# Kernel optimization log

Hardware: AMD Instinct MI355X
Metric: run time of the kernel (lower is better)

## Reference

```python
import jax, jax.numpy as jnp
import numpy as np
from jax import lax

N_CLS = 3
ALPHA = 2
NMS = True


def _make_level(key, B, A, D, H, W, P, counts):
    k1, k2, k3, k4, k5 = jax.random.split(key, 5)
    C = N_CLS * A
    logit = jax.random.normal(k1, (B, C, D, H, W), dtype=jnp.float32)
    # valid positive coords use d,h,w >= 1 so padded writes to (0,0,0,0) never collide
    a = jax.random.randint(k2, (B, P), 0, A)
    d = jax.random.randint(k3, (B, P), 1, D)
    h = jax.random.randint(k4, (B, P), 1, H)
    w = jax.random.randint(k5, (B, P), 1, W)
    labels = jax.random.randint(jax.random.fold_in(key, 7), (B, P), 0, N_CLS)
    valid = jnp.arange(P)[None, :] < jnp.asarray(counts)[:, None]  # [B,P]
    coord = jnp.stack([a, d, h, w], axis=-1)
    coord = jnp.where(valid[..., None], coord, -1).astype(jnp.int32)
    # ground-truth prob map: -1 = negative, class id (float) at positive voxels
    prob_gt = -jnp.ones((B, A, D, H, W), dtype=jnp.float32)
    cs = jnp.where(valid[..., None], coord, 0)
    b_idx = jnp.arange(B)[:, None]
    vals = jnp.where(valid, labels.astype(jnp.float32), -1.0)
    prob_gt = prob_gt.at[b_idx, cs[..., 0], cs[..., 1], cs[..., 2], cs[..., 3]].set(vals)
    return logit, prob_gt, coord


def setup_inputs() -> dict:
    key = jax.random.key(0)
    kA, kB = jax.random.split(key)
    logit0, prob_gt0, coord0 = _make_level(kA, 4, 3, 64, 64, 64, 128, [128, 64, 32, 0])
    logit1, prob_gt1, coord1 = _make_level(kB, 4, 3, 32, 32, 32, 128, [64, 16, 8, 128])
    weight_cls = jnp.array([1.0, 1.5, 2.0], dtype=jnp.float32)
    return {
        "logit0": logit0, "logit1": logit1,
        "prob_gt0": prob_gt0, "prob_gt1": prob_gt1,
        "coord0": coord0, "coord1": coord1,
        "weight_cls": weight_cls,
    }


def _level_loss(logit, prob_gt, coord_gt, weight_cls):
    B, C, D, H, W = logit.shape
    A = C // N_CLS
    logit = logit.reshape(B, N_CLS, A, D, H, W)
    logp = jax.nn.log_softmax(logit, axis=1)
    nll = -logp                      # [B,N_cls,A,D,H,W]
    prob = jnp.exp(logp)
    nll_neg = nll[:, 0]              # [B,A,D,H,W]
    prob_neg = prob[:, 0]
    negmask = (prob_gt == -1).astype(logit.dtype)
    if NMS:
        mp = lax.reduce_window(nll_neg, -jnp.inf, lax.max,
                               (1, 1, 3, 3, 3), (1, 1, 1, 1, 1),
                               [(0, 0), (0, 0), (1, 1), (1, 1), (1, 1)])
        negmask = negmask * lax.stop_gradient((mp == nll_neg).astype(logit.dtype))
    w_neg = (1.0 - lax.stop_gradient(prob_neg)) ** ALPHA * negmask
    loss_neg = jnp.sum(nll_neg * w_neg)
    count_neg = jnp.sum(w_neg)
    # positives: ragged coord gather, masked instead of per-sample python loop
    valid = coord_gt[:, :, 0] > -1                       # [B,P]
    c = jnp.where(valid[..., None], coord_gt, 0)         # safe coords
    a, d, h, w = c[..., 0], c[..., 1], c[..., 2], c[..., 3]
    b_idx = jnp.arange(B)[:, None]
    cls = prob_gt[b_idx, a, d, h, w].astype(jnp.int32)   # class id at positives
    cls = jnp.where(valid, cls, 0)
    p_t = prob[b_idx, cls, a, d, h, w]
    nll_t = nll[b_idx, cls, a, d, h, w]
    w_pos = ((1.0 - lax.stop_gradient(p_t)) ** ALPHA
             * weight_cls[cls] * valid.astype(logit.dtype))
    loss_pos = jnp.sum(nll_t * w_pos)
    count_pos = jnp.sum(w_pos)
    return loss_pos, loss_neg, count_pos, count_neg


def reference(logit0, logit1, prob_gt0, prob_gt1, coord0, coord1, weight_cls):
    lp0, ln0, cp0, cn0 = _level_loss(logit0, prob_gt0, coord0, weight_cls)
    lp1, ln1, cp1, cn1 = _level_loss(logit1, prob_gt1, coord1, weight_cls)
    return jnp.stack([lp0 + lp1, ln0 + ln1, cp0 + cp1, cn0 + cn1])
```

## Files before the change

### kernel.cpp

```cpp
#include <hip/hip_runtime.h>
#include <math.h>

#define NEG_INF (-INFINITY)

__device__ __forceinline__ float nll3(float l0, float l1, float l2) {
    float m = fmaxf(l0, fmaxf(l1, l2));
    float e0 = __expf(l0 - m);
    float e1 = __expf(l1 - m);
    float e2 = __expf(l2 - m);
    return __logf(e0 + e1 + e2) - (l0 - m);
}

__device__ __forceinline__ float4 fmax4(float4 a, float4 b) {
    return make_float4(fmaxf(a.x, b.x), fmaxf(a.y, b.y),
                       fmaxf(a.z, b.z), fmaxf(a.w, b.w));
}

template<int W, int HT, int ZT, int D, int H>
__device__ void neg_block(int ub, int tid,
                          const float* __restrict__ logit,
                          const float* __restrict__ pg,
                          float2* __restrict__ slot,
                          float* lds, float2* red) {
    constexpr int LQ = W / 4;
    constexpr int SR = W + 4;
    constexpr int SROWS = HT + 2;
    constexpr int QS = SROWS * LQ;
    constexpr int HW = H * W;
    constexpr int ZTI = D / ZT;
    constexpr int HTI = H / HT;
    constexpr int NLL_SZ = SROWS * SR;
    constexpr int HV_OFF = 3 * NLL_SZ;
    constexpr int HV_SZ = HT * SR;

    int t = ub;
    const int ht = t % HTI; t /= HTI;
    const int zt = t % ZTI; t /= ZTI;
    const int ba = t;
    const int a = ba % 3, b = ba / 3;
    const int z0 = zt * ZT, h0 = ht * HT;

    const long S = (long)D * HW;
    const long cs = 3 * S;
    const float* lb  = logit + ((long)b * 9 + a) * S;
    const float* pgb = pg + (long)ba * S;

    const int er = tid / LQ;
    const int q  = tid % LQ;
    const int lane = tid & 63;
    const int l_er = er * SR + 4 * q;
    const int po = (h0 + er) * W + 4 * q;

    int roff[2]; bool rok[2];
#pragma unroll
    for (int r = 0; r < 2; ++r) {
        const int k = tid + 256 * r;
        const int row = k / LQ, qq = k % LQ;
        const int h = h0 - 1 + row;
        rok[r]  = (k < QS) && (h >= 0) && (h < H);
        roff[r] = min(max(h, 0), H - 1) * W + 4 * qq;
    }

    float4 rA[2][3] = {}, rB[2][3] = {};
    float4 pgA = {}, pgB = {};
    bool pvA, pvB = false;

    auto issue = [&](float4 (&rg)[2][3], int zp) -> bool {
        const bool pv = (zp >= 0) && (zp < D);
        if (pv) {
#pragma unroll
            for (int r = 0; r < 2; ++r) {
                if (tid + 256 * r < QS) {
                    const float* p = lb + (long)zp * HW + roff[r];
                    rg[r][0] = *(const float4*)p;
                    rg[r][1] = *(const float4*)(p + cs);
                    rg[r][2] = *(const float4*)(p + 2 * cs);
                }
            }
        }
        return pv;
    };

    pvA = issue(rA, z0 - 1);

    float loss = 0.f, cnt = 0.f;

#pragma unroll
    for (int zi = 0; zi <= ZT + 1; ++zi) {
        const int zc = z0 - 1 + zi;
        if (zi <= ZT) pvB = issue(rB, zc + 1);
        if (zi >= 1 && zi <= ZT)
            pgB = *(const float4*)(pgb + (long)zc * HW + po);

        {
            float* nb = lds + (zi % 3) * NLL_SZ;
#pragma unroll
            for (int r = 0; r < 2; ++r) {
                const int k = tid + 256 * r;
                if (k < QS) {
                    const int row = k / LQ, qq = k % LQ;
                    const bool ok = pvA && rok[r];
                    float4 n;
                    n.x = ok ? nll3(rA[r][0].x, rA[r][1].x, rA[r][2].x) : NEG_INF;
                    n.y = ok ? nll3(rA[r][0].y, rA[r][1].y, rA[r][2].y) : NEG_INF;
                    n.z = ok ? nll3(rA[r][0].z, rA[r][1].z, rA[r][2].z) : NEG_INF;
                    n.w = ok ? nll3(rA[r][0].w, rA[r][1].w, rA[r][2].w) : NEG_INF;
                    *(float4*)(nb + row * SR + 4 * qq) = n;
                }
            }
        }
        __syncthreads();

        {
            const float* nb = lds + (zi % 3) * NLL_SZ;
            float* hb = lds + HV_OFF + (zi % 3) * HV_SZ;
            float4 v0 = *(const float4*)(nb + l_er);
            float4 v1 = *(const float4*)(nb + l_er + SR);
            float4 v2 = *(const float4*)(nb + l_er + 2 * SR);
            float4 vm = fmax4(v0, fmax4(v1, v2));
            float le = __shfl(vm.w, lane - 1);
            float re = __shfl(vm.x, lane + 1);
            le = (q == 0)      ? NEG_INF : le;
            re = (q == LQ - 1) ? NEG_INF : re;
            float4 hv;
            hv.x = fmaxf(le,   fmaxf(vm.x, vm.y));
            hv.y = fmaxf(vm.x, fmaxf(vm.y, vm.z));
            hv.z = fmaxf(vm.y, fmaxf(vm.z, vm.w));
            hv.w = fmaxf(vm.z, fmaxf(vm.w, re));
            *(float4*)(hb + l_er) = hv;
        }
        __syncthreads();

        if (zi >= 2) {
            const float* nbm = lds + ((zi - 1) % 3) * NLL_SZ;
            const float* hb0 = lds + HV_OFF + ((zi - 2) % 3) * HV_SZ;
            const float* hb1 = lds + HV_OFF + ((zi - 1) % 3) * HV_SZ;
            const float* hb2 = lds + HV_OFF + (zi % 3) * HV_SZ;
            float4 nc = *(const float4*)(nbm + l_er + SR);
            float4 m  = fmax4(*(const float4*)(hb0 + l_er),
                        fmax4(*(const float4*)(hb1 + l_er),
                              *(const float4*)(hb2 + l_er)));
            const float pgv[4] = {pgA.x, pgA.y, pgA.z, pgA.w};
            const float ncv[4] = {nc.x, nc.y, nc.z, nc.w};
            const float mv[4]  = {m.x, m.y, m.z, m.w};
#pragma unroll
            for (int i = 0; i < 4; ++i) {
                if (pgv[i] == -1.0f && mv[i] == ncv[i]) {
                    float pn = __expf(-ncv[i]);
                    float wn = (1.f - pn) * (1.f - pn);
                    loss += ncv[i] * wn;
                    cnt  += wn;
                }
            }
        }

        pvA = pvB;
#pragma unroll
        for (int r = 0; r < 2; ++r)
#pragma unroll
            for (int c = 0; c < 3; ++c) rA[r][c] = rB[r][c];
        pgA = pgB;
    }

#pragma unroll
    for (int off = 32; off > 0; off >>= 1) {
        loss += __shfl_down(loss, off);
        cnt  += __shfl_down(cnt, off);
    }
    if (lane == 0) red[tid >> 6] = make_float2(loss, cnt);
    __syncthreads();
    if (tid == 0) {
        float sx = 0.f, sy = 0.f;
#pragma unroll
        for (int i = 0; i < 4; ++i) { sx += red[i].x; sy += red[i].y; }
        *slot = make_float2(sx, sy);
    }
}

__device__ void pos_wave8(int sub, int lane,
                          const float* __restrict__ logit,
                          const float* __restrict__ prob_gt,
                          const int* __restrict__ coord,
                          const float* __restrict__ wcls,
                          float2* __restrict__ slot,
                          int D, int H, int W) {
    const int A = 3, P = 128;
    const long S = (long)D * H * W;
    const int i = sub * 64 + lane;
    const int b = i / P;
    const int* c = coord + (long)i * 4;
    const int a = c[0];
    float loss = 0.f, cnt = 0.f;
    if (a > -1) {
        const int d = c[1], h = c[2], w = c[3];
        const long s = ((long)d * H + h) * W + w;
        const int cls = (int)prob_gt[((long)b * A + a) * S + s];
        const float* lp = logit + ((long)b * 3 * A + a) * S + s;
        float l0 = lp[0];
        float l1 = lp[(long)A * S];
        float l2 = lp[2L * A * S];
        float m = fmaxf(l0, fmaxf(l1, l2));
        float e0 = __expf(l0 - m);
        float e1 = __expf(l1 - m);
        float e2 = __expf(l2 - m);
        float lsum = __logf(e0 + e1 + e2);
        float lc = (cls == 0) ? l0 : ((cls == 1) ? l1 : l2);
        float lpc = (lc - m) - lsum;
        float pt = __expf(lpc);
        float wp = (1.f - pt) * (1.f - pt) * wcls[cls];
        loss = (-lpc) * wp;
        cnt = wp;
    }
#pragma unroll
    for (int off = 32; off > 0; off >>= 1) {
        loss += __shfl_down(loss, off);
        cnt  += __shfl_down(cnt, off);
    }
    if (lane == 0) *slot = make_float2(loss, cnt);
}

#define NB0 768
#define NB1 96
#define NBNEG (NB0 + NB1)
#define NBP 4
#define TOTAL_BLOCKS (NBNEG + NBP)
#define NWP 16

__global__ __launch_bounds__(256)
void mega_kernel(const float* __restrict__ logit0,
                 const float* __restrict__ logit1,
                 const float* __restrict__ pg0,
                 const float* __restrict__ pg1,
                 const int* __restrict__ coord0,
                 const int* __restrict__ coord1,
                 const float* __restrict__ wcls,
                 float2* __restrict__ ws) {
    __shared__ float lds[7128];
    __shared__ float2 red[4];
    const int bid = blockIdx.x;
    const int tid = threadIdx.x;
    float2* wsneg = ws;
    float2* wspos = ws + NBNEG;
    if (bid < NB0) {
        neg_block<64, 16, 4, 64, 64>(bid, tid, logit0, pg0, wsneg + bid, lds, red);
    } else if (bid < NBNEG) {
        neg_block<32, 32, 4, 32, 32>(bid - NB0, tid, logit1, pg1, wsneg + bid, lds, red);
    } else {
        const int gwl = (bid - NBNEG) * 4 + (tid >> 6);
        const int lane = tid & 63;
        if (gwl < 8)
            pos_wave8(gwl, lane, logit0, pg0, coord0, wcls, wspos + gwl, 64, 64, 64);
        else
            pos_wave8(gwl - 8, lane, logit1, pg1, coord1, wcls, wspos + gwl, 32, 32, 32);
    }
}

__global__ __launch_bounds__(1024)
void final_reduce(const float2* __restrict__ ws, float* __restrict__ out) {
    const float2* wsneg = ws;
    const float2* wspos = ws + NBNEG;
    float ln = 0.f, cn = 0.f, lp = 0.f, cp = 0.f;
    for (int i = threadIdx.x; i < NBNEG; i += 1024) {
        float2 v = wsneg[i]; ln += v.x; cn += v.y;
    }
    if (threadIdx.x < NWP) {
        float2 v = wspos[threadIdx.x]; lp = v.x; cp = v.y;
    }
#pragma unroll
    for (int off = 32; off > 0; off >>= 1) {
        ln += __shfl_down(ln, off); cn += __shfl_down(cn, off);
        lp += __shfl_down(lp, off); cp += __shfl_down(cp, off);
    }
    __shared__ float s[16][4];
    const int wv = threadIdx.x >> 6;
    if ((threadIdx.x & 63) == 0) {
        s[wv][0] = ln; s[wv][1] = cn; s[wv][2] = lp; s[wv][3] = cp;
    }
    __syncthreads();
    if (threadIdx.x == 0) {
        float a = 0.f, b = 0.f, c = 0.f, d = 0.f;
#pragma unroll
        for (int i = 0; i < 16; ++i) {
            a += s[i][0]; b += s[i][1]; c += s[i][2]; d += s[i][3];
        }
        out[0] = c;
        out[1] = a;
        out[2] = d;
        out[3] = b;
    }
}

extern "C" void kernel_launch(void* const* d_in, const int* in_sizes, int n_in,
                              void* d_out, int out_size, void* d_ws, size_t ws_size,
                              hipStream_t stream) {
    const float* logit0   = (const float*)d_in[0];
    const float* logit1   = (const float*)d_in[1];
    const float* prob_gt0 = (const float*)d_in[2];
    const float* prob_gt1 = (const float*)d_in[3];
    const int*   coord0   = (const int*)d_in[4];
    const int*   coord1   = (const int*)d_in[5];
    const float* wcls     = (const float*)d_in[6];
    float* out = (float*)d_out;
    float2* ws = (float2*)d_ws;

    mega_kernel<<<TOTAL_BLOCKS, 256, 0, stream>>>(
        logit0, logit1, prob_gt0, prob_gt1, coord0, coord1, wcls, ws);
    final_reduce<<<1, 1024, 0, stream>>>(ws, out);
}
```

Measured before the change: 105.3 us.

## Stage logits into LDS via async global_load_lds and keep pooling in registers

The negative-loss blocks now copy the three class-logit planes for each z-slice straight into double-buffered LDS with global_load_lds, instead of loading through registers and writing nll values to LDS. Each thread recomputes the nll for its three h-rows from LDS. The horizontal-max results for the previous two slices stay in registers, which cuts the LDS traffic and drops the per-slice barriers from two to one. Out-of-range h and z are clamped to edge rows, which leaves the 3x3x3 max unchanged. In exchange, each thread does roughly three times as many exp/log evaluations, and correctness now depends on the async LDS loads being complete at the barrier.

```diff
diff --git a/kernel.cpp b/kernel.cpp
--- a/kernel.cpp
+++ b/kernel.cpp
@@ -1,5 +1,6 @@
 #include <hip/hip_runtime.h>
 #include <math.h>
+#include <stdint.h>
 
 #define NEG_INF (-INFINITY)
 
@@ -14,6 +15,12 @@
 __device__ __forceinline__ float4 fmax4(float4 a, float4 b) {
     return make_float4(fmaxf(a.x, b.x), fmaxf(a.y, b.y),
                        fmaxf(a.z, b.z), fmaxf(a.w, b.w));
+}
+
+__device__ __forceinline__ void gld16(const float* g, float* l) {
+    __builtin_amdgcn_global_load_lds(
+        (__attribute__((address_space(1))) void*)(g),
+        (__attribute__((address_space(3))) void*)(l), 16, 0, 0);
 }
 
 template<int W, int HT, int ZT, int D, int H>
@@ -23,15 +30,16 @@
                           float2* __restrict__ slot,
                           float* lds, float2* red) {
     constexpr int LQ = W / 4;
-    constexpr int SR = W + 4;
     constexpr int SROWS = HT + 2;
     constexpr int QS = SROWS * LQ;
+    constexpr int QSF = QS * 4;
+    constexpr int PLF = 3 * QSF;
+    constexpr int TQ = 3 * QS;
+    constexpr int NRND = (TQ + 63) / 64;
+    constexpr int RPW = (NRND + 3) / 4;
     constexpr int HW = H * W;
     constexpr int ZTI = D / ZT;
     constexpr int HTI = H / HT;
-    constexpr int NLL_SZ = SROWS * SR;
-    constexpr int HV_OFF = 3 * NLL_SZ;
-    constexpr int HV_SZ = HT * SR;
 
     int t = ub;
     const int ht = t % HTI; t /= HTI;
@@ -45,104 +53,89 @@
     const float* lb  = logit + ((long)b * 9 + a) * S;
     const float* pgb = pg + (long)ba * S;
 
+    const int lane = tid & 63;
+    const int wid  = tid >> 6;
+
+    const float* gsrc[RPW];
+    int ldso[RPW];
+#pragma unroll
+    for (int r = 0; r < RPW; ++r) {
+        int rt = wid + 4 * r;
+        if (rt >= NRND) rt = wid;
+        const int base = min(rt * 64, TQ - 64);
+        const int j = base + lane;
+        const int c = j / QS;
+        const int k = j - c * QS;
+        const int row = k / LQ, qq = k - row * LQ;
+        const int h = min(max(h0 - 1 + row, 0), H - 1);
+        gsrc[r] = lb + (long)c * cs + h * W + 4 * qq;
+        ldso[r] = j * 4;
+    }
+
     const int er = tid / LQ;
     const int q  = tid % LQ;
-    const int lane = tid & 63;
-    const int l_er = er * SR + 4 * q;
     const int po = (h0 + er) * W + 4 * q;
-
-    int roff[2]; bool rok[2];
-#pragma unroll
-    for (int r = 0; r < 2; ++r) {
-        const int k = tid + 256 * r;
-        const int row = k / LQ, qq = k % LQ;
-        const int h = h0 - 1 + row;
-        rok[r]  = (k < QS) && (h >= 0) && (h < H);
-        roff[r] = min(max(h, 0), H - 1) * W + 4 * qq;
-    }
-
-    float4 rA[2][3] = {}, rB[2][3] = {};
-    float4 pgA = {}, pgB = {};
-    bool pvA, pvB = false;
-
-    auto issue = [&](float4 (&rg)[2][3], int zp) -> bool {
-        const bool pv = (zp >= 0) && (zp < D);
-        if (pv) {
-#pragma unroll
-            for (int r = 0; r < 2; ++r) {
-                if (tid + 256 * r < QS) {
-                    const float* p = lb + (long)zp * HW + roff[r];
-                    rg[r][0] = *(const float4*)p;
-                    rg[r][1] = *(const float4*)(p + cs);
-                    rg[r][2] = *(const float4*)(p + 2 * cs);
-                }
-            }
-        }
-        return pv;
+    const int cb = er * W + 4 * q;
+
+    auto stage = [&](int zp, int s) {
+        const long zoff = (long)min(max(zp, 0), D - 1) * HW;
+        float* dst = lds + s * PLF;
+#pragma unroll
+        for (int r = 0; r < RPW; ++r)
+            gld16(gsrc[r] + zoff, dst + ldso[r]);
     };
 
-    pvA = issue(rA, z0 - 1);
-
+    stage(z0 - 1, 0);
+    __syncthreads();
+
+    float4 hv0 = make_float4(NEG_INF, NEG_INF, NEG_INF, NEG_INF);
+    float4 hv1 = hv0;
+    float4 ncp = hv0;
+    float4 pgA = make_float4(0.f, 0.f, 0.f, 0.f), pgB = pgA;
     float loss = 0.f, cnt = 0.f;
 
 #pragma unroll
     for (int zi = 0; zi <= ZT + 1; ++zi) {
         const int zc = z0 - 1 + zi;
-        if (zi <= ZT) pvB = issue(rB, zc + 1);
+
+        if (zi <= ZT) stage(z0 + zi, (zi + 1) & 1);
         if (zi >= 1 && zi <= ZT)
             pgB = *(const float4*)(pgb + (long)zc * HW + po);
 
+        float4 hv2, ncc;
         {
-            float* nb = lds + (zi % 3) * NLL_SZ;
-#pragma unroll
-            for (int r = 0; r < 2; ++r) {
-                const int k = tid + 256 * r;
-                if (k < QS) {
-                    const int row = k / LQ, qq = k % LQ;
-                    const bool ok = pvA && rok[r];
-                    float4 n;
-                    n.x = ok ? nll3(rA[r][0].x, rA[r][1].x, rA[r][2].x) : NEG_INF;
-                    n.y = ok ? nll3(rA[r][0].y, rA[r][1].y, rA[r][2].y) : NEG_INF;
-                    n.z = ok ? nll3(rA[r][0].z, rA[r][1].z, rA[r][2].z) : NEG_INF;
-                    n.w = ok ? nll3(rA[r][0].w, rA[r][1].w, rA[r][2].w) : NEG_INF;
-                    *(float4*)(nb + row * SR + 4 * qq) = n;
-                }
+            const float* sb = lds + (zi & 1) * PLF;
+            float4 vm = make_float4(NEG_INF, NEG_INF, NEG_INF, NEG_INF);
+            ncc = vm;
+#pragma unroll
+            for (int j = 0; j < 3; ++j) {
+                const float* rp = sb + cb + j * W;
+                float4 a0 = *(const float4*)(rp);
+                float4 a1 = *(const float4*)(rp + QSF);
+                float4 a2 = *(const float4*)(rp + 2 * QSF);
+                float4 n;
+                n.x = nll3(a0.x, a1.x, a2.x);
+                n.y = nll3(a0.y, a1.y, a2.y);
+                n.z = nll3(a0.z, a1.z, a2.z);
+                n.w = nll3(a0.w, a1.w, a2.w);
+                if (j == 1) ncc = n;
+                vm = fmax4(vm, n);
             }
-        }
-        __syncthreads();
-
-        {
-            const float* nb = lds + (zi % 3) * NLL_SZ;
-            float* hb = lds + HV_OFF + (zi % 3) * HV_SZ;
-            float4 v0 = *(const float4*)(nb + l_er);
-            float4 v1 = *(const float4*)(nb + l_er + SR);
-            float4 v2 = *(const float4*)(nb + l_er + 2 * SR);
-            float4 vm = fmax4(v0, fmax4(v1, v2));
             float le = __shfl(vm.w, lane - 1);
             float re = __shfl(vm.x, lane + 1);
             le = (q == 0)      ? NEG_INF : le;
             re = (q == LQ - 1) ? NEG_INF : re;
-            float4 hv;
-            hv.x = fmaxf(le,   fmaxf(vm.x, vm.y));
-            hv.y = fmaxf(vm.x, fmaxf(vm.y, vm.z));
-            hv.z = fmaxf(vm.y, fmaxf(vm.z, vm.w));
-            hv.w = fmaxf(vm.z, fmaxf(vm.w, re));
-            *(float4*)(hb + l_er) = hv;
+            hv2.x = fmaxf(le,   fmaxf(vm.x, vm.y));
+            hv2.y = fmaxf(vm.x, fmaxf(vm.y, vm.z));
+            hv2.z = fmaxf(vm.y, fmaxf(vm.z, vm.w));
+            hv2.w = fmaxf(vm.z, fmaxf(vm.w, re));
         }
-        __syncthreads();
 
         if (zi >= 2) {
-            const float* nbm = lds + ((zi - 1) % 3) * NLL_SZ;
-            const float* hb0 = lds + HV_OFF + ((zi - 2) % 3) * HV_SZ;
-            const float* hb1 = lds + HV_OFF + ((zi - 1) % 3) * HV_SZ;
-            const float* hb2 = lds + HV_OFF + (zi % 3) * HV_SZ;
-            float4 nc = *(const float4*)(nbm + l_er + SR);
-            float4 m  = fmax4(*(const float4*)(hb0 + l_er),
-                        fmax4(*(const float4*)(hb1 + l_er),
-                              *(const float4*)(hb2 + l_er)));
+            float4 m3 = fmax4(hv0, fmax4(hv1, hv2));
             const float pgv[4] = {pgA.x, pgA.y, pgA.z, pgA.w};
-            const float ncv[4] = {nc.x, nc.y, nc.z, nc.w};
-            const float mv[4]  = {m.x, m.y, m.z, m.w};
+            const float ncv[4] = {ncp.x, ncp.y, ncp.z, ncp.w};
+            const float mv[4]  = {m3.x, m3.y, m3.z, m3.w};
 #pragma unroll
             for (int i = 0; i < 4; ++i) {
                 if (pgv[i] == -1.0f && mv[i] == ncv[i]) {
@@ -154,12 +147,9 @@
             }
         }
 
-        pvA = pvB;
-#pragma unroll
-        for (int r = 0; r < 2; ++r)
-#pragma unroll
-            for (int c = 0; c < 3; ++c) rA[r][c] = rB[r][c];
-        pgA = pgB;
+        hv0 = hv1; hv1 = hv2; ncp = ncc; pgA = pgB;
+
+        __syncthreads();
     }
 
 #pragma unroll
@@ -167,7 +157,7 @@
         loss += __shfl_down(loss, off);
         cnt  += __shfl_down(cnt, off);
     }
-    if (lane == 0) red[tid >> 6] = make_float2(loss, cnt);
+    if (lane == 0) red[wid] = make_float2(loss, cnt);
     __syncthreads();
     if (tid == 0) {
         float sx = 0.f, sy = 0.f;
@@ -235,7 +225,7 @@
                  const int* __restrict__ coord1,
                  const float* __restrict__ wcls,
                  float2* __restrict__ ws) {
-    __shared__ float lds[7128];
+    __shared__ __align__(16) float lds[6912];
     __shared__ float2 red[4];
     const int bid = blockIdx.x;
     const int tid = threadIdx.x;
```

After: 109.6 us. 4.1% more time.
